# Optimization experiments

Hardware: AMD Instinct MI355X
Metric: run time of the kernel (lower is better)

Reference implementation:

```python
import jax, jax.numpy as jnp
import numpy as np

N_NODES = 50000
N_EDGES = 800000
IN_CH = 128
HID = 32
HEADS = 4
OUT_CH = 10
N_GRAPHS = 64
NEG_SLOPE = 0.2  # PyG GATConv default


def setup_inputs() -> dict:
    key = jax.random.key(0)
    ks = jax.random.split(key, 16)
    d = {}
    d["x"] = jax.random.normal(ks[0], (N_NODES, IN_CH), dtype=jnp.float32)
    d["edge_index"] = jax.random.randint(ks[1], (2, N_EDGES), 0, N_NODES, dtype=jnp.int64)
    d["batch"] = jnp.sort(jax.random.randint(ks[2], (N_NODES,), 0, N_GRAPHS, dtype=jnp.int64))
    s1 = 1.0 / np.sqrt(IN_CH)
    s2 = 1.0 / np.sqrt(HEADS * HID)
    d["W1"] = jax.random.normal(ks[3], (IN_CH, HEADS * HID), dtype=jnp.float32) * s1
    d["att_src1"] = jax.random.normal(ks[4], (HEADS, HID), dtype=jnp.float32) * s2
    d["att_dst1"] = jax.random.normal(ks[5], (HEADS, HID), dtype=jnp.float32) * s2
    d["b1"] = jnp.zeros((HEADS * HID,), dtype=jnp.float32)
    d["W2"] = jax.random.normal(ks[6], (HEADS * HID, HEADS * HID), dtype=jnp.float32) * s2
    d["att_src2"] = jax.random.normal(ks[7], (HEADS, HID), dtype=jnp.float32) * s2
    d["att_dst2"] = jax.random.normal(ks[8], (HEADS, HID), dtype=jnp.float32) * s2
    d["b2"] = jnp.zeros((HEADS * HID,), dtype=jnp.float32)
    d["w_lin"] = jax.random.normal(ks[9], (HEADS * HID, OUT_CH), dtype=jnp.float32) * s2
    d["b_lin"] = jnp.zeros((OUT_CH,), dtype=jnp.float32)
    return d


def _gat_conv(x, src, dst, W, att_src, att_dst, bias):
    # x: [N, Fin] -> h: [N, H, C]
    h = (x @ W).reshape(N_NODES, HEADS, HID)
    a_src = jnp.sum(h * att_src, axis=-1)  # [N, H]
    a_dst = jnp.sum(h * att_dst, axis=-1)  # [N, H]
    e = jax.nn.leaky_relu(a_src[src] + a_dst[dst], NEG_SLOPE)  # [E, H]
    # segment softmax over incoming edges of each destination node
    e_max = jax.ops.segment_max(e, dst, num_segments=N_NODES)  # [N, H]
    e_exp = jnp.exp(e - e_max[dst])
    denom = jax.ops.segment_sum(e_exp, dst, num_segments=N_NODES)  # [N, H]
    alpha = e_exp / denom[dst]  # [E, H]
    # weighted scatter-add aggregation
    out = jax.ops.segment_sum(alpha[:, :, None] * h[src], dst, num_segments=N_NODES)
    return out.reshape(N_NODES, HEADS * HID) + bias


def reference(x, edge_index, batch, W1, att_src1, att_dst1, b1,
              W2, att_src2, att_dst2, b2, w_lin, b_lin):
    # PyG GATConv adds self loops by default
    loops = jnp.arange(N_NODES, dtype=edge_index.dtype)
    src = jnp.concatenate([edge_index[0], loops])
    dst = jnp.concatenate([edge_index[1], loops])

    h = jax.nn.relu(_gat_conv(x, src, dst, W1, att_src1, att_dst1, b1))
    h = jax.nn.relu(_gat_conv(h, src, dst, W2, att_src2, att_dst2, b2))

    # global mean pool over graphs
    sums = jax.ops.segment_sum(h, batch, num_segments=N_GRAPHS)  # [G, H*C]
    counts = jax.ops.segment_sum(jnp.ones((N_NODES,), dtype=h.dtype), batch,
                                 num_segments=N_GRAPHS)
    pooled = sums / jnp.maximum(counts, 1.0)[:, None]

    # dropout is identity in eval mode
    return pooled @ w_lin + b_lin
```

## Files before the change

### kernel.cpp

```cpp
#include <hip/hip_runtime.h>
#include <hip/hip_bf16.h>
#include <math.h>

constexpr int NN = 50000;
constexpr int NE = 800000;
constexpr int ET = NE + NN;
constexpr int FH = 128;
constexpr int NHEAD = 4;
constexpr int NG = 64;
constexpr int OC = 10;

constexpr int NBK = (NN + 255) >> 8;
constexpr int EPB = 4000;
constexpr int HBLK = NE / EPB;

constexpr int WKP = 136;
constexpr int WPLANE = 128 * WKP;

constexpr int GEMM1_GRID = (NN + 255) / 256;
constexpr int GEMM2_GRID = (NN + 63) / 64;

typedef __attribute__((ext_vector_type(8))) short short8;
typedef __attribute__((ext_vector_type(4))) float f32x4;

__device__ inline ushort f2bf_bits(float f) {
    union { __hip_bfloat16 h; ushort u; } c;
    c.h = __float2bfloat16(f);
    return c.u;
}

__global__ __launch_bounds__(256) void pack_kernel(const float* __restrict__ W1,
                                                   const float* __restrict__ W2,
                                                   ushort* __restrict__ wt) {
    int idx = blockIdx.x * 256 + threadIdx.x;
    int layer = idx >> 14;
    int k = (idx >> 7) & 127;
    int n = idx & 127;
    const float* W = layer ? W2 : W1;
    float f = W[k * 128 + n];
    ushort hb = f2bf_bits(f);
    union { ushort u; __hip_bfloat16 h; } c; c.u = hb;
    float lo = f - __bfloat162float(c.h);
    ushort* base = wt + layer * 2 * WPLANE;
    base[n * WKP + k] = hb;
    base[WPLANE + n * WKP + k] = f2bf_bits(lo);
}

#define GEMM_EPILOGUE()                                                          \
    float as_[8], ad_[8];                                                        \
    _Pragma("unroll")                                                            \
    for (int t = 0; t < 8; ++t) {                                                \
        as_[t] = att_s[t * 16 + l16];                                            \
        ad_[t] = att_d[t * 16 + l16];                                            \
    }                                                                            \
    float hs[4][4], hd[4][4];                                                    \
    _Pragma("unroll")                                                            \
    for (int r = 0; r < 4; ++r) {                                                \
        int grow = row0 + quad * 4 + r;                                          \
        bool okr = (grow < NN);                                                  \
        _Pragma("unroll")                                                        \
        for (int h = 0; h < 4; ++h) {                                            \
            hs[r][h] = acc[2*h][r] * as_[2*h] + acc[2*h+1][r] * as_[2*h+1];      \
            hd[r][h] = acc[2*h][r] * ad_[2*h] + acc[2*h+1][r] * ad_[2*h+1];      \
        }                                                                        \
        if (okr) {                                                               \
            _Pragma("unroll")                                                    \
            for (int t = 0; t < 8; ++t)                                          \
                Hb[(size_t)grow * FH + t * 16 + l16] = __float2bfloat16(acc[t][r]); \
        }                                                                        \
    }                                                                            \
    _Pragma("unroll")                                                            \
    for (int o = 1; o < 16; o <<= 1) {                                           \
        _Pragma("unroll")                                                        \
        for (int r = 0; r < 4; ++r)                                              \
            _Pragma("unroll")                                                    \
            for (int h = 0; h < 4; ++h) {                                        \
                hs[r][h] += __shfl_xor(hs[r][h], o);                             \
                hd[r][h] += __shfl_xor(hd[r][h], o);                             \
            }                                                                    \
    }                                                                            \
    if (l16 == 0) {                                                              \
        _Pragma("unroll")                                                        \
        for (int r = 0; r < 4; ++r) {                                            \
            int grow = row0 + quad * 4 + r;                                      \
            if (grow < NN) {                                                     \
                *(float4*)&a_src[grow * NHEAD] = make_float4(hs[r][0], hs[r][1], hs[r][2], hs[r][3]); \
                *(float4*)&a_dst[grow * NHEAD] = make_float4(hd[r][0], hd[r][1], hd[r][2], hd[r][3]); \
            }                                                                    \
        }                                                                        \
    }

__global__ __launch_bounds__(1024) void fused_gemm_hist_kernel(
    const int* __restrict__ ei, int* __restrict__ blockHist,
    const float* __restrict__ A, const ushort* __restrict__ wt,
    const float* __restrict__ att_s, const float* __restrict__ att_d,
    __hip_bfloat16* __restrict__ Hb, float* __restrict__ a_src, float* __restrict__ a_dst)
{
    __shared__ ushort Wlds[2 * WPLANE];
    const int tid = threadIdx.x;

    if (blockIdx.x >= GEMM1_GRID) {
        const int blk = blockIdx.x - GEMM1_GRID;
        int* hist = (int*)Wlds;
        if (tid < NBK) hist[tid] = 0;
        __syncthreads();
        const int e0 = blk * EPB;
        if (tid < EPB / 4) {
            int4 d4 = *(const int4*)(ei + NE + e0 + 4 * tid);
            atomicAdd(&hist[d4.x >> 8], 1);
            atomicAdd(&hist[d4.y >> 8], 1);
            atomicAdd(&hist[d4.z >> 8], 1);
            atomicAdd(&hist[d4.w >> 8], 1);
        }
        __syncthreads();
        if (tid < NBK) blockHist[tid * HBLK + blk] = hist[tid];
        return;
    }

    {
        const uint4* s = (const uint4*)wt;
        uint4* d = (uint4*)Wlds;
        for (int i = tid; i < 2 * WPLANE / 8; i += 1024) d[i] = s[i];
    }
    __syncthreads();

    const int wave = tid >> 6;
    const int lane = tid & 63;
    const int quad = lane >> 4;
    const int l16 = lane & 15;
    const int row0 = blockIdx.x * 256 + wave * 16;

    f32x4 acc[8];
#pragma unroll
    for (int t = 0; t < 8; ++t) acc[t] = (f32x4){0.f, 0.f, 0.f, 0.f};

    int arow = row0 + l16; if (arow >= NN) arow = NN - 1;
    const float* ap = A + (size_t)arow * FH + quad * 8;

#pragma unroll
    for (int kc = 0; kc < 4; ++kc) {
        float4 x0 = *(const float4*)(ap + kc * 32);
        float4 x1 = *(const float4*)(ap + kc * 32 + 4);
        float av[8] = {x0.x, x0.y, x0.z, x0.w, x1.x, x1.y, x1.z, x1.w};
        short8 ah, al;
#pragma unroll
        for (int j = 0; j < 8; ++j) {
            ushort hb = f2bf_bits(av[j]);
            union { ushort u; __hip_bfloat16 h; } c; c.u = hb;
            float lo = av[j] - __bfloat162float(c.h);
            ah[j] = (short)hb;
            al[j] = (short)f2bf_bits(lo);
        }
        const int kof = kc * 32 + quad * 8;
#pragma unroll
        for (int t = 0; t < 8; ++t) {
            const ushort* wp = &Wlds[(t * 16 + l16) * WKP + kof];
            short8 wh = *(const short8*)wp;
            short8 wl = *(const short8*)(wp + WPLANE);
            acc[t] = __builtin_amdgcn_mfma_f32_16x16x32_bf16(ah, wh, acc[t], 0, 0, 0);
            acc[t] = __builtin_amdgcn_mfma_f32_16x16x32_bf16(al, wh, acc[t], 0, 0, 0);
            acc[t] = __builtin_amdgcn_mfma_f32_16x16x32_bf16(ah, wl, acc[t], 0, 0, 0);
        }
    }
    GEMM_EPILOGUE()
}

__global__ __launch_bounds__(256) void scanA_kernel(int* __restrict__ bh,
                                                    int* __restrict__ bsumB) {
    __shared__ int sd[256];
    const int b = blockIdx.x, t = threadIdx.x;
    int v = (t < HBLK) ? bh[b * HBLK + t] : 0;
    sd[t] = v; __syncthreads();
#pragma unroll
    for (int o = 1; o < 256; o <<= 1) {
        int u = (t >= o) ? sd[t - o] : 0;
        __syncthreads();
        sd[t] += u;
        __syncthreads();
    }
    if (t < HBLK) bh[b * HBLK + t] = sd[t] - v;
    if (t == 255) bsumB[b] = sd[255];
}

__global__ __launch_bounds__(256) void scanB_kernel(const int* __restrict__ bsumB,
                                                    int* __restrict__ ebase,
                                                    int* __restrict__ offs) {
    __shared__ int sd[256];
    const int t = threadIdx.x;
    int v = (t < NBK) ? bsumB[t] : 0;
    sd[t] = v; __syncthreads();
#pragma unroll
    for (int o = 1; o < 256; o <<= 1) {
        int u = (t >= o) ? sd[t - o] : 0;
        __syncthreads();
        sd[t] += u;
        __syncthreads();
    }
    if (t < NBK) ebase[t] = sd[t] - v;
    if (t == NBK - 1) ebase[NBK] = sd[t];
    if (t == 0) offs[NN] = ET;
}

__global__ __launch_bounds__(1024) void bucket_scatter_kernel(
    const int* __restrict__ ei, const int* __restrict__ bh,
    const int* __restrict__ ebase, int2* __restrict__ ebuf) {
    __shared__ int cur[NBK];
    const int tid = threadIdx.x;
    const int blk = blockIdx.x;
    for (int i = tid; i < NBK; i += 1024) cur[i] = ebase[i] + bh[i * HBLK + blk];
    __syncthreads();
    const int e0 = blk * EPB;
    if (tid < EPB / 4) {
        int4 d4 = *(const int4*)(ei + NE + e0 + 4 * tid);
        int4 s4 = *(const int4*)(ei + e0 + 4 * tid);
        int ds[4] = {d4.x, d4.y, d4.z, d4.w};
        int ss[4] = {s4.x, s4.y, s4.z, s4.w};
#pragma unroll
        for (int j = 0; j < 4; ++j) {
            int pos = atomicAdd(&cur[ds[j] >> 8], 1);
            ebuf[pos] = make_int2(ss[j], ds[j]);
        }
    }
}

__global__ __launch_bounds__(256) void bucket_csr_kernel(
    const int2* __restrict__ ebuf, const int* __restrict__ ebase,
    int* __restrict__ offs, int* __restrict__ csrc) {
    __shared__ int hist[256];
    __shared__ int sd[256];
    __shared__ int cur[256];
    const int b = blockIdx.x, t = threadIdx.x;
    const int lo = b << 8;
    int psz = NN - lo; if (psz > 256) psz = 256;
    const int e0 = ebase[b], e1 = ebase[b + 1];

    hist[t] = 0;
    __syncthreads();
    for (int k = e0 + t; k < e1; k += 256) {
        int2 e = ebuf[k];
        atomicAdd(&hist[e.y - lo], 1);
    }
    __syncthreads();
    const int d = hist[t];
    sd[t] = d; __syncthreads();
#pragma unroll
    for (int o = 1; o < 256; o <<= 1) {
        int u = (t >= o) ? sd[t - o] : 0;
        __syncthreads();
        sd[t] += u;
        __syncthreads();
    }
    const int ex = sd[t] - d;
    if (t < psz) {
        const int node = lo + t;
        const int o = e0 + ex + node;
        offs[node] = o;
        cur[t] = o;
        csrc[o + d] = node;
    }
    __syncthreads();
    for (int k = e0 + t; k < e1; k += 256) {
        int2 e = ebuf[k];
        int pos = atomicAdd(&cur[e.y - lo], 1);
        csrc[pos] = e.x;
    }
}

__global__ __launch_bounds__(256) void gemm_att_bf16_kernel(
    const __hip_bfloat16* __restrict__ A, const ushort* __restrict__ wt,
    const float* __restrict__ att_s, const float* __restrict__ att_d,
    __hip_bfloat16* __restrict__ Hb, float* __restrict__ a_src, float* __restrict__ a_dst)
{
    __shared__ ushort Wlds[2 * WPLANE];
    const int tid = threadIdx.x;
    {
        const uint4* s = (const uint4*)wt;
        uint4* d = (uint4*)Wlds;
        for (int i = tid; i < 2 * WPLANE / 8; i += 256) d[i] = s[i];
    }
    __syncthreads();

    const int wave = tid >> 6;
    const int lane = tid & 63;
    const int quad = lane >> 4;
    const int l16 = lane & 15;
    const int row0 = blockIdx.x * 64 + wave * 16;

    f32x4 acc[8];
#pragma unroll
    for (int t = 0; t < 8; ++t) acc[t] = (f32x4){0.f, 0.f, 0.f, 0.f};

    int arow = row0 + l16; if (arow >= NN) arow = NN - 1;
    const __hip_bfloat16* ap = A + (size_t)arow * FH + quad * 8;

#pragma unroll
    for (int kc = 0; kc < 4; ++kc) {
        short8 ah = *(const short8*)(ap + kc * 32);
        const int kof = kc * 32 + quad * 8;
#pragma unroll
        for (int t = 0; t < 8; ++t) {
            const ushort* wp = &Wlds[(t * 16 + l16) * WKP + kof];
            short8 wh = *(const short8*)wp;
            short8 wl = *(const short8*)(wp + WPLANE);
            acc[t] = __builtin_amdgcn_mfma_f32_16x16x32_bf16(ah, wh, acc[t], 0, 0, 0);
            acc[t] = __builtin_amdgcn_mfma_f32_16x16x32_bf16(ah, wl, acc[t], 0, 0, 0);
        }
    }
    GEMM_EPILOGUE()
}

__global__ __launch_bounds__(256) void gat_agg_kernel(
    const __hip_bfloat16* __restrict__ Hb, const float* __restrict__ asrc,
    const float* __restrict__ adst, const int* __restrict__ offs,
    const int* __restrict__ csrc, const float* __restrict__ bias,
    __hip_bfloat16* __restrict__ out)
{
    __shared__ float2 wbuf[4][4][65];
    const int wid = threadIdx.x >> 6;
    const int lane = threadIdx.x & 63;
    const int n = blockIdx.x * 4 + wid;
    if (n >= NN) return;

    const int beg = offs[n], end = offs[n + 1];
    const int hB = lane & 3;
    const int eslot = lane >> 2;
    const float adB = adst[n * NHEAD + hB];
    float2* wrow = wbuf[wid][hB];
    const int es = lane >> 4;
    const int fs = lane & 15;
    const int hC = fs >> 2;
    const int f8 = fs * 8;
    const float2* crow = wbuf[wid][hC];

    float d = 0.f;
    float acc[8];
#pragma unroll
    for (int i = 0; i < 8; ++i) acc[i] = 0.f;

    for (int cs = beg; cs < end; cs += 64) {
        int ce = end - cs; if (ce > 64) ce = 64;
        for (int k = eslot; k < ce; k += 16) {
            int s = csrc[cs + k];
            float e = asrc[s * NHEAD + hB] + adB;
            e = e > 0.f ? e : 0.2f * e;
            float w = __expf(e);
            d += w;
            wrow[k] = make_float2(w, __int_as_float(s));
        }
        __asm__ volatile("s_waitcnt lgkmcnt(0)" ::: "memory");
        const int n8 = (ce + 7) >> 3;
        for (int p = 0; p < n8; ++p) {
            int eA = 8 * p + es;
            int eB = eA + 4;
            float2 wsA = crow[eA < ce ? eA : 0];
            float2 wsB = crow[eB < ce ? eB : 0];
            float wA = eA < ce ? wsA.x : 0.f;
            float wB = eB < ce ? wsB.x : 0.f;
            int sA = __float_as_int(wsA.y);
            int sB = __float_as_int(wsB.y);
            union { uint4 u; __hip_bfloat162 b[4]; } cvA, cvB;
            cvA.u = *(const uint4*)&Hb[(size_t)sA * FH + f8];
            cvB.u = *(const uint4*)&Hb[(size_t)sB * FH + f8];
#pragma unroll
            for (int i = 0; i < 4; ++i) {
                float2 hA = __bfloat1622float2(cvA.b[i]);
                float2 hB2 = __bfloat1622float2(cvB.b[i]);
                acc[2 * i]     = fmaf(wA, hA.x, acc[2 * i]);
                acc[2 * i + 1] = fmaf(wA, hA.y, acc[2 * i + 1]);
                acc[2 * i]     = fmaf(wB, hB2.x, acc[2 * i]);
                acc[2 * i + 1] = fmaf(wB, hB2.y, acc[2 * i + 1]);
            }
        }
    }
#pragma unroll
    for (int o = 4; o < 64; o <<= 1) d += __shfl_xor(d, o);
#pragma unroll
    for (int i = 0; i < 8; ++i) {
        acc[i] += __shfl_xor(acc[i], 16);
        acc[i] += __shfl_xor(acc[i], 32);
    }
    const float inv = 1.0f / __shfl(d, hC);
    if (es == 0) {
        union { ushort u8[8]; uint4 u; } pk;
#pragma unroll
        for (int i = 0; i < 8; ++i) {
            float v = fmaxf(fmaf(acc[i], inv, bias[f8 + i]), 0.f);
            pk.u8[i] = f2bf_bits(v);
        }
        *(uint4*)&out[(size_t)n * FH + f8] = pk.u;
    }
}

__global__ __launch_bounds__(256) void pool_kernel(
    const __hip_bfloat16* __restrict__ X, const int* __restrict__ batch,
    float* __restrict__ sums, int* __restrict__ cnts)
{
    const int g = blockIdx.x;
    const int t = threadIdx.x;
    int a = 0, b = NN;
    while (a < b) { int m = (a + b) >> 1; if (batch[m] < g) a = m + 1; else b = m; }
    const int gs = a;
    b = NN;
    while (a < b) { int m = (a + b) >> 1; if (batch[m] <= g) a = m + 1; else b = m; }
    const int ge = a;

    const int rg = t >> 4;
    const int l16 = t & 15;
    float acc[8];
#pragma unroll
    for (int i = 0; i < 8; ++i) acc[i] = 0.f;
    for (int r = gs + rg; r < ge; r += 16) {
        union { uint4 u; __hip_bfloat162 bb[4]; } cv;
        cv.u = *(const uint4*)&X[(size_t)r * FH + l16 * 8];
#pragma unroll
        for (int i = 0; i < 4; ++i) {
            float2 f = __bfloat1622float2(cv.bb[i]);
            acc[2 * i]     += f.x;
            acc[2 * i + 1] += f.y;
        }
    }
    __shared__ float red[16][128];
#pragma unroll
    for (int i = 0; i < 8; ++i) red[rg][l16 * 8 + i] = acc[i];
    __syncthreads();
    if (t < 128) {
        float s = 0.f;
#pragma unroll
        for (int j = 0; j < 16; ++j) s += red[j][t];
        sums[g * FH + t] = s;
    }
    if (t == 0) cnts[g] = ge - gs;
}

__global__ void final_kernel(const float* __restrict__ sums, const int* __restrict__ cnts,
                             const float* __restrict__ wl, const float* __restrict__ bl,
                             float* __restrict__ out)
{
    const int t = threadIdx.x;
    if (t >= NG * OC) return;
    const int g = t / OC, o = t % OC;
    float invc = 1.0f / fmaxf((float)cnts[g], 1.0f);
    float acc = 0.f;
    for (int k = 0; k < FH; ++k)
        acc = fmaf(sums[g * FH + k], wl[k * OC + o], acc);
    out[t] = acc * invc + bl[o];
}

extern "C" void kernel_launch(void* const* d_in, const int* in_sizes, int n_in,
                              void* d_out, int out_size, void* d_ws, size_t ws_size,
                              hipStream_t stream) {
    const float* x       = (const float*)d_in[0];
    const int*   ei      = (const int*)d_in[1];
    const int*   batch   = (const int*)d_in[2];
    const float* W1      = (const float*)d_in[3];
    const float* as1     = (const float*)d_in[4];
    const float* ad1     = (const float*)d_in[5];
    const float* b1      = (const float*)d_in[6];
    const float* W2      = (const float*)d_in[7];
    const float* as2     = (const float*)d_in[8];
    const float* ad2     = (const float*)d_in[9];
    const float* b2      = (const float*)d_in[10];
    const float* wlin    = (const float*)d_in[11];
    const float* blin    = (const float*)d_in[12];
    float* out = (float*)d_out;

    __hip_bfloat16* hbuf = (__hip_bfloat16*)d_ws;
    __hip_bfloat16* abuf = hbuf + (size_t)NN * FH;
    float* asrc  = (float*)(abuf + (size_t)NN * FH);
    float* adst  = asrc + (size_t)NN * NHEAD;
    float* sums  = adst + (size_t)NN * NHEAD;
    int*   cnts  = (int*)(sums + NG * FH);
    int* offs    = cnts + NG;
    int* csrc    = offs + NN + 1;
    int2* ebuf   = (int2*)(((uintptr_t)(csrc + ET) + 7) & ~(uintptr_t)7);
    int* bh      = (int*)(ebuf + NE);
    int* bsumB   = bh + NBK * HBLK;
    int* ebase   = bsumB + NBK;
    ushort* wt   = (ushort*)(((uintptr_t)(ebase + NBK + 1) + 15) & ~(uintptr_t)15);

    pack_kernel<<<128, 256, 0, stream>>>(W1, W2, wt);

    fused_gemm_hist_kernel<<<GEMM1_GRID + HBLK, 1024, 0, stream>>>(
        ei, bh, x, wt, as1, ad1, hbuf, asrc, adst);

    scanA_kernel<<<NBK, 256, 0, stream>>>(bh, bsumB);
    scanB_kernel<<<1, 256, 0, stream>>>(bsumB, ebase, offs);
    bucket_scatter_kernel<<<HBLK, 1024, 0, stream>>>(ei, bh, ebase, ebuf);
    bucket_csr_kernel<<<NBK, 256, 0, stream>>>(ebuf, ebase, offs, csrc);

    const int agg_grid = (NN + 3) / 4;

    gat_agg_kernel<<<agg_grid, 256, 0, stream>>>(hbuf, asrc, adst, offs, csrc, b1, abuf);
    gemm_att_bf16_kernel<<<GEMM2_GRID, 256, 0, stream>>>(abuf, wt + 2 * WPLANE, as2, ad2, hbuf, asrc, adst);
    gat_agg_kernel<<<agg_grid, 256, 0, stream>>>(hbuf, asrc, adst, offs, csrc, b2, abuf);

    pool_kernel<<<NG, 256, 0, stream>>>(abuf, batch, sums, cnts);
    final_kernel<<<1, NG * OC, 0, stream>>>(sums, cnts, wlin, blin, out);
}
```

Baseline: 253.2 us.

## Fold weight packing, scans and final linear into neighboring kernels; vectorize attention

```diff
diff --git a/kernel.cpp b/kernel.cpp
--- a/kernel.cpp
+++ b/kernel.cpp
@@ -27,23 +27,6 @@
     union { __hip_bfloat16 h; ushort u; } c;
     c.h = __float2bfloat16(f);
     return c.u;
-}
-
-__global__ __launch_bounds__(256) void pack_kernel(const float* __restrict__ W1,
-                                                   const float* __restrict__ W2,
-                                                   ushort* __restrict__ wt) {
-    int idx = blockIdx.x * 256 + threadIdx.x;
-    int layer = idx >> 14;
-    int k = (idx >> 7) & 127;
-    int n = idx & 127;
-    const float* W = layer ? W2 : W1;
-    float f = W[k * 128 + n];
-    ushort hb = f2bf_bits(f);
-    union { ushort u; __hip_bfloat16 h; } c; c.u = hb;
-    float lo = f - __bfloat162float(c.h);
-    ushort* base = wt + layer * 2 * WPLANE;
-    base[n * WKP + k] = hb;
-    base[WPLANE + n * WKP + k] = f2bf_bits(lo);
 }
 
 #define GEMM_EPILOGUE()                                                          \
@@ -92,7 +75,8 @@
 
 __global__ __launch_bounds__(1024) void fused_gemm_hist_kernel(
     const int* __restrict__ ei, int* __restrict__ blockHist,
-    const float* __restrict__ A, const ushort* __restrict__ wt,
+    const float* __restrict__ A, const float* __restrict__ W1,
+    const float* __restrict__ W2, ushort* __restrict__ wt,
     const float* __restrict__ att_s, const float* __restrict__ att_d,
     __hip_bfloat16* __restrict__ Hb, float* __restrict__ a_src, float* __restrict__ a_dst)
 {
@@ -112,15 +96,29 @@
             atomicAdd(&hist[d4.z >> 8], 1);
             atomicAdd(&hist[d4.w >> 8], 1);
         }
+        if (blk < 64 && tid < 256) {
+            int idx = blk * 256 + tid;
+            int k = idx >> 7, n = idx & 127;
+            float f = W2[idx];
+            ushort hb = f2bf_bits(f);
+            union { ushort u; __hip_bfloat16 h; } c; c.u = hb;
+            float lo = f - __bfloat162float(c.h);
+            wt[n * WKP + k] = hb;
+            wt[WPLANE + n * WKP + k] = f2bf_bits(lo);
+        }
         __syncthreads();
         if (tid < NBK) blockHist[tid * HBLK + blk] = hist[tid];
         return;
     }
 
-    {
-        const uint4* s = (const uint4*)wt;
-        uint4* d = (uint4*)Wlds;
-        for (int i = tid; i < 2 * WPLANE / 8; i += 1024) d[i] = s[i];
+    for (int i = tid; i < FH * 128; i += 1024) {
+        int k = i >> 7, n = i & 127;
+        float f = W1[i];
+        ushort hb = f2bf_bits(f);
+        union { ushort u; __hip_bfloat16 h; } c; c.u = hb;
+        float lo = f - __bfloat162float(c.h);
+        Wlds[n * WKP + k] = hb;
+        Wlds[WPLANE + n * WKP + k] = f2bf_bits(lo);
     }
     __syncthreads();
 
@@ -165,11 +163,18 @@
     GEMM_EPILOGUE()
 }
 
-__global__ __launch_bounds__(256) void scanA_kernel(int* __restrict__ bh,
-                                                    int* __restrict__ bsumB) {
+__global__ __launch_bounds__(256) void scanAB_kernel(const int* __restrict__ bh,
+                                                     int* __restrict__ bstart,
+                                                     int* __restrict__ ebase,
+                                                     int* __restrict__ offs) {
     __shared__ int sd[256];
+    __shared__ int bprefix;
     const int b = blockIdx.x, t = threadIdx.x;
-    int v = (t < HBLK) ? bh[b * HBLK + t] : 0;
+    int v = 0;
+    if (t < NBK) {
+        const int* p = bh + t * HBLK;
+        for (int i = 0; i < HBLK; ++i) v += p[i];
+    }
     sd[t] = v; __syncthreads();
 #pragma unroll
     for (int o = 1; o < 256; o <<= 1) {
@@ -178,17 +183,17 @@
         sd[t] += u;
         __syncthreads();
     }
-    if (t < HBLK) bh[b * HBLK + t] = sd[t] - v;
-    if (t == 255) bsumB[b] = sd[255];
-}
-
-__global__ __launch_bounds__(256) void scanB_kernel(const int* __restrict__ bsumB,
-                                                    int* __restrict__ ebase,
-                                                    int* __restrict__ offs) {
-    __shared__ int sd[256];
-    const int t = threadIdx.x;
-    int v = (t < NBK) ? bsumB[t] : 0;
-    sd[t] = v; __syncthreads();
+    if (t == b) bprefix = sd[t] - v;
+    if (b == 0) {
+        if (t < NBK) ebase[t] = sd[t] - v;
+        if (t == NBK - 1) ebase[NBK] = sd[t];
+        if (t == 0) offs[NN] = ET;
+    }
+    __syncthreads();
+    const int base = bprefix;
+    __syncthreads();
+    int c = (t < HBLK) ? bh[b * HBLK + t] : 0;
+    sd[t] = c; __syncthreads();
 #pragma unroll
     for (int o = 1; o < 256; o <<= 1) {
         int u = (t >= o) ? sd[t - o] : 0;
@@ -196,18 +201,16 @@
         sd[t] += u;
         __syncthreads();
     }
-    if (t < NBK) ebase[t] = sd[t] - v;
-    if (t == NBK - 1) ebase[NBK] = sd[t];
-    if (t == 0) offs[NN] = ET;
+    if (t < HBLK) bstart[b * HBLK + t] = base + sd[t] - c;
 }
 
 __global__ __launch_bounds__(1024) void bucket_scatter_kernel(
-    const int* __restrict__ ei, const int* __restrict__ bh,
-    const int* __restrict__ ebase, int2* __restrict__ ebuf) {
+    const int* __restrict__ ei, const int* __restrict__ bstart,
+    int2* __restrict__ ebuf) {
     __shared__ int cur[NBK];
     const int tid = threadIdx.x;
     const int blk = blockIdx.x;
-    for (int i = tid; i < NBK; i += 1024) cur[i] = ebase[i] + bh[i * HBLK + blk];
+    for (int i = tid; i < NBK; i += 1024) cur[i] = bstart[i * HBLK + blk];
     __syncthreads();
     const int e0 = blk * EPB;
     if (tid < EPB / 4) {
@@ -315,49 +318,50 @@
     const int* __restrict__ csrc, const float* __restrict__ bias,
     __hip_bfloat16* __restrict__ out)
 {
-    __shared__ float2 wbuf[4][4][65];
+    __shared__ float ebl[4][64][5];
     const int wid = threadIdx.x >> 6;
     const int lane = threadIdx.x & 63;
     const int n = blockIdx.x * 4 + wid;
-    if (n >= NN) return;
 
     const int beg = offs[n], end = offs[n + 1];
-    const int hB = lane & 3;
-    const int eslot = lane >> 2;
-    const float adB = adst[n * NHEAD + hB];
-    float2* wrow = wbuf[wid][hB];
+    const float4 ad4 = *(const float4*)&adst[n * NHEAD];
     const int es = lane >> 4;
     const int fs = lane & 15;
     const int hC = fs >> 2;
     const int f8 = fs * 8;
-    const float2* crow = wbuf[wid][hC];
-
-    float d = 0.f;
+    float (*erow)[5] = ebl[wid];
+
+    float dsum[4] = {0.f, 0.f, 0.f, 0.f};
     float acc[8];
 #pragma unroll
     for (int i = 0; i < 8; ++i) acc[i] = 0.f;
 
     for (int cs = beg; cs < end; cs += 64) {
         int ce = end - cs; if (ce > 64) ce = 64;
-        for (int k = eslot; k < ce; k += 16) {
-            int s = csrc[cs + k];
-            float e = asrc[s * NHEAD + hB] + adB;
-            e = e > 0.f ? e : 0.2f * e;
-            float w = __expf(e);
-            d += w;
-            wrow[k] = make_float2(w, __int_as_float(s));
+        if (lane < ce) {
+            int s = csrc[cs + lane];
+            float4 av = *(const float4*)&asrc[s * NHEAD];
+            float e0 = av.x + ad4.x; e0 = e0 > 0.f ? e0 : 0.2f * e0;
+            float e1 = av.y + ad4.y; e1 = e1 > 0.f ? e1 : 0.2f * e1;
+            float e2 = av.z + ad4.z; e2 = e2 > 0.f ? e2 : 0.2f * e2;
+            float e3 = av.w + ad4.w; e3 = e3 > 0.f ? e3 : 0.2f * e3;
+            float w0 = __expf(e0), w1 = __expf(e1), w2 = __expf(e2), w3 = __expf(e3);
+            dsum[0] += w0; dsum[1] += w1; dsum[2] += w2; dsum[3] += w3;
+            erow[lane][0] = w0; erow[lane][1] = w1;
+            erow[lane][2] = w2; erow[lane][3] = w3;
+            erow[lane][4] = __int_as_float(s);
         }
         __asm__ volatile("s_waitcnt lgkmcnt(0)" ::: "memory");
         const int n8 = (ce + 7) >> 3;
         for (int p = 0; p < n8; ++p) {
             int eA = 8 * p + es;
             int eB = eA + 4;
-            float2 wsA = crow[eA < ce ? eA : 0];
-            float2 wsB = crow[eB < ce ? eB : 0];
-            float wA = eA < ce ? wsA.x : 0.f;
-            float wB = eB < ce ? wsB.x : 0.f;
-            int sA = __float_as_int(wsA.y);
-            int sB = __float_as_int(wsB.y);
+            int iA = eA < ce ? eA : 0;
+            int iB = eB < ce ? eB : 0;
+            float wA = eA < ce ? erow[iA][hC] : 0.f;
+            float wB = eB < ce ? erow[iB][hC] : 0.f;
+            int sA = __float_as_int(erow[iA][4]);
+            int sB = __float_as_int(erow[iB][4]);
             union { uint4 u; __hip_bfloat162 b[4]; } cvA, cvB;
             cvA.u = *(const uint4*)&Hb[(size_t)sA * FH + f8];
             cvB.u = *(const uint4*)&Hb[(size_t)sB * FH + f8];
@@ -373,13 +377,16 @@
         }
     }
 #pragma unroll
-    for (int o = 4; o < 64; o <<= 1) d += __shfl_xor(d, o);
+    for (int o = 1; o < 64; o <<= 1) {
+#pragma unroll
+        for (int h = 0; h < 4; ++h) dsum[h] += __shfl_xor(dsum[h], o);
+    }
 #pragma unroll
     for (int i = 0; i < 8; ++i) {
         acc[i] += __shfl_xor(acc[i], 16);
         acc[i] += __shfl_xor(acc[i], 32);
     }
-    const float inv = 1.0f / __shfl(d, hC);
+    const float inv = 1.0f / dsum[hC];
     if (es == 0) {
         union { ushort u8[8]; uint4 u; } pk;
 #pragma unroll
@@ -391,9 +398,10 @@
     }
 }
 
-__global__ __launch_bounds__(256) void pool_kernel(
+__global__ __launch_bounds__(256) void pool_final_kernel(
     const __hip_bfloat16* __restrict__ X, const int* __restrict__ batch,
-    float* __restrict__ sums, int* __restrict__ cnts)
+    const float* __restrict__ wl, const float* __restrict__ bl,
+    float* __restrict__ out)
 {
     const int g = blockIdx.x;
     const int t = threadIdx.x;
@@ -420,6 +428,7 @@
         }
     }
     __shared__ float red[16][128];
+    __shared__ float pl[128];
 #pragma unroll
     for (int i = 0; i < 8; ++i) red[rg][l16 * 8 + i] = acc[i];
     __syncthreads();
@@ -427,23 +436,16 @@
         float s = 0.f;
 #pragma unroll
         for (int j = 0; j < 16; ++j) s += red[j][t];
-        sums[g * FH + t] = s;
-    }
-    if (t == 0) cnts[g] = ge - gs;
-}
-
-__global__ void final_kernel(const float* __restrict__ sums, const int* __restrict__ cnts,
-                             const float* __restrict__ wl, const float* __restrict__ bl,
-                             float* __restrict__ out)
-{
-    const int t = threadIdx.x;
-    if (t >= NG * OC) return;
-    const int g = t / OC, o = t % OC;
-    float invc = 1.0f / fmaxf((float)cnts[g], 1.0f);
-    float acc = 0.f;
-    for (int k = 0; k < FH; ++k)
-        acc = fmaf(sums[g * FH + k], wl[k * OC + o], acc);
-    out[t] = acc * invc + bl[o];
+        pl[t] = s;
+    }
+    __syncthreads();
+    if (t < OC) {
+        float invc = 1.0f / fmaxf((float)(ge - gs), 1.0f);
+        float a2 = 0.f;
+        for (int k = 0; k < FH; ++k)
+            a2 = fmaf(pl[k], wl[k * OC + t], a2);
+        out[g * OC + t] = a2 * invc + bl[t];
+    }
 }
 
 extern "C" void kernel_launch(void* const* d_in, const int* in_sizes, int n_in,
@@ -468,32 +470,26 @@
     __hip_bfloat16* abuf = hbuf + (size_t)NN * FH;
     float* asrc  = (float*)(abuf + (size_t)NN * FH);
     float* adst  = asrc + (size_t)NN * NHEAD;
-    float* sums  = adst + (size_t)NN * NHEAD;
-    int*   cnts  = (int*)(sums + NG * FH);
-    int* offs    = cnts + NG;
+    int* offs    = (int*)(adst + (size_t)NN * NHEAD);
     int* csrc    = offs + NN + 1;
     int2* ebuf   = (int2*)(((uintptr_t)(csrc + ET) + 7) & ~(uintptr_t)7);
     int* bh      = (int*)(ebuf + NE);
-    int* bsumB   = bh + NBK * HBLK;
-    int* ebase   = bsumB + NBK;
+    int* bstart  = bh + NBK * HBLK;
+    int* ebase   = bstart + NBK * HBLK;
     ushort* wt   = (ushort*)(((uintptr_t)(ebase + NBK + 1) + 15) & ~(uintptr_t)15);
 
-    pack_kernel<<<128, 256, 0, stream>>>(W1, W2, wt);
-
     fused_gemm_hist_kernel<<<GEMM1_GRID + HBLK, 1024, 0, stream>>>(
-        ei, bh, x, wt, as1, ad1, hbuf, asrc, adst);
-
-    scanA_kernel<<<NBK, 256, 0, stream>>>(bh, bsumB);
-    scanB_kernel<<<1, 256, 0, stream>>>(bsumB, ebase, offs);
-    bucket_scatter_kernel<<<HBLK, 1024, 0, stream>>>(ei, bh, ebase, ebuf);
+        ei, bh, x, W1, W2, wt, as1, ad1, hbuf, asrc, adst);
+
+    scanAB_kernel<<<NBK, 256, 0, stream>>>(bh, bstart, ebase, offs);
+    bucket_scatter_kernel<<<HBLK, 1024, 0, stream>>>(ei, bstart, ebuf);
     bucket_csr_kernel<<<NBK, 256, 0, stream>>>(ebuf, ebase, offs, csrc);
 
-    const int agg_grid = (NN + 3) / 4;
+    const int agg_grid = NN / 4;
 
     gat_agg_kernel<<<agg_grid, 256, 0, stream>>>(hbuf, asrc, adst, offs, csrc, b1, abuf);
-    gemm_att_bf16_kernel<<<GEMM2_GRID, 256, 0, stream>>>(abuf, wt + 2 * WPLANE, as2, ad2, hbuf, asrc, adst);
+    gemm_att_bf16_kernel<<<GEMM2_GRID, 256, 0, stream>>>(abuf, wt, as2, ad2, hbuf, asrc, adst);
     gat_agg_kernel<<<agg_grid, 256, 0, stream>>>(hbuf, asrc, adst, offs, csrc, b2, abuf);
 
-    pool_kernel<<<NG, 256, 0, stream>>>(abuf, batch, sums, cnts);
-    final_kernel<<<1, NG * OC, 0, stream>>>(sums, cnts, wlin, blin, out);
-}
+    pool_final_kernel<<<NG, 256, 0, stream>>>(abuf, batch, wlin, blin, out);
+}
```

Result: no change. 253.3 us (+0.1%).
